# Kernel tuning notes

Measured on AMD Instinct MI355X. Metric: run time of the kernel, lower is better.

The kernel has to match this reference:

```python
import jax, jax.numpy as jnp
import numpy as np
import math

D = 768
H = 12
DH = D // H
L = 2
EPS = 1e-12
NEG = -10000.0


def layer_norm(x, w, b):
    u = jnp.mean(x, axis=-1, keepdims=True)
    s = jnp.mean((x - u) ** 2, axis=-1, keepdims=True)
    return w * ((x - u) / jnp.sqrt(s + EPS)) + b


def mha(q_in, k_in, v_in, mask, qw, qb, kw, kb, vw, vb):
    # q_in: (B,Lq,D); k_in/v_in: (B,Lk,D); mask: (B,Lq,Lk) or (B,1,Lk)
    B, Lq, _ = q_in.shape
    def proj(x, w, b):
        y = x @ w.T + b
        return y.reshape(x.shape[0], x.shape[1], H, DH).transpose(0, 2, 1, 3)
    q = proj(q_in, qw, qb)  # (B,H,Lq,DH)
    k = proj(k_in, kw, kb)
    v = proj(v_in, vw, vb)
    scores = jnp.einsum('bhqd,bhkd->bhqk', q, k) / math.sqrt(DH)
    scores = scores + (1.0 - mask[:, None]) * NEG  # additive mask, (B,1,Lq,Lk) broadcast
    probs = jax.nn.softmax(scores, axis=-1)
    ctx = jnp.einsum('bhqk,bhkd->bhqd', probs, v)
    return ctx.transpose(0, 2, 1, 3).reshape(B, Lq, D)


def setup_inputs() -> dict:
    key = jax.random.key(0)
    ks = jax.random.split(key, 8)
    B, Lt, Lv = 8, 1024, 512
    inp = {
        'dec_hidden_states': jax.random.normal(ks[0], (B, Lt, D), jnp.float32),
        'dec_mask': jnp.ones((B, Lt), jnp.float32),
        'enc_outputs': jax.random.normal(ks[1], (B, Lv, D), jnp.float32),
        'enc_mask': jnp.ones((B, Lv), jnp.float32),
    }
    wkeys = jax.random.split(ks[2], 7)
    names = ['sa_qw', 'sa_kw', 'sa_vw', 'ca_qw', 'ca_kw', 'ca_vw', 'out_w']
    for n, k in zip(names, wkeys):
        inp[n] = 0.02 * jax.random.normal(k, (L, D, D), jnp.float32)
    for n in ['sa_qb', 'sa_kb', 'sa_vb', 'ca_qb', 'ca_kb', 'ca_vb', 'out_b', 'n1_b', 'n2_b', 'n3_b']:
        inp[n] = jnp.zeros((L, D), jnp.float32)
    for n in ['n1_w', 'n2_w', 'n3_w']:
        inp[n] = jnp.ones((L, D), jnp.float32)
    return inp


def reference(dec_hidden_states, dec_mask, enc_outputs, enc_mask,
              sa_qw, sa_qb, sa_kw, sa_kb, sa_vw, sa_vb, n1_w, n1_b,
              ca_qw, ca_qb, ca_kw, ca_kb, ca_vw, ca_vb, n2_w, n2_b,
              out_w, out_b, n3_w, n3_b):
    Lt = dec_hidden_states.shape[1]
    causal = jnp.tril(jnp.ones((Lt, Lt), dec_mask.dtype))
    self_mask = dec_mask[:, None, :] * causal[None]        # (B,Lt,Lt)
    cross_mask = enc_mask[:, None, :]                      # (B,1,Lv)

    params = (sa_qw, sa_qb, sa_kw, sa_kb, sa_vw, sa_vb, n1_w, n1_b,
              ca_qw, ca_qb, ca_kw, ca_kb, ca_vw, ca_vb, n2_w, n2_b,
              out_w, out_b, n3_w, n3_b)

    def body(x, p):
        (qw, qb, kw, kb, vw, vb, w1, b1,
         cqw, cqb, ckw, ckb, cvw, cvb, w2, b2,
         ow, ob, w3, b3) = p
        a = mha(x, x, x, self_mask, qw, qb, kw, kb, vw, vb)
        x1 = layer_norm(a + x, w1, b1)
        c = mha(x1, enc_outputs, enc_outputs, cross_mask, cqw, cqb, ckw, ckb, cvw, cvb)
        x2 = layer_norm(x1 + c, w2, b2)
        # BertOutput called with (x2, x2): LN(dense(x2) + x2)
        y = layer_norm(x2 @ ow.T + ob + x2, w3, b3)
        return y, None

    out, _ = jax.lax.scan(body, dec_hidden_states, params)
    return out
```

## Files before the change

kernel.cpp:

```cpp
#include <hip/hip_runtime.h>
#include <hip/hip_bf16.h>

#define DMODEL 768
#define NH 12
#define DH 64
#define NEGC -10000.0f

#define AS1 __attribute__((address_space(1)))
#define AS3 __attribute__((address_space(3)))

typedef __bf16 bf16_t;
typedef __bf16 bf16x8 __attribute__((ext_vector_type(8)));
typedef float f32x4 __attribute__((ext_vector_type(4)));

__device__ __forceinline__ f32x4 mfma16(bf16x8 a, bf16x8 b, f32x4 c) {
    return __builtin_amdgcn_mfma_f32_16x16x32_bf16(a, b, c, 0, 0, 0);
}

__device__ __forceinline__ void gl_lds16(const bf16_t* g, void* l) {
    __builtin_amdgcn_global_load_lds((const AS1 void*)g, (AS3 void*)l, 16, 0, 0);
}

__global__ void probe_kernel(const unsigned int* m, int* flag) {
    *flag = (m[0] == 0x3F803F80u) ? 1 : 0;
}

__device__ __forceinline__ void cvt_group(const void* src, bf16_t* dst, int g, int isbf16) {
    if (isbf16) {
        ((bf16x8*)dst)[g] = ((const bf16x8*)src)[g];
    } else {
        const float* s = (const float*)src + (size_t)g * 8;
        bf16x8 v;
#pragma unroll
        for (int i = 0; i < 8; i++) v[i] = (bf16_t)s[i];
        ((bf16x8*)dst)[g] = v;
    }
}

__global__ __launch_bounds__(256) void cvt_kernel(const void* src, bf16_t* dst,
                                                  const int* flag, int n) {
    int g = blockIdx.x * 256 + threadIdx.x;
    if (g * 8 >= n) return;
    cvt_group(src, dst, g, *flag);
}

__global__ __launch_bounds__(256) void cvt7_kernel(
    const void* s0, const void* s1, const void* s2, const void* s3,
    const void* s4, const void* s5, const void* s6,
    bf16_t* dst, const int* flag)
{
    const void* srcs[7] = {s0, s1, s2, s3, s4, s5, s6};
    const void* src = srcs[blockIdx.y];
    bf16_t* d = dst + (size_t)blockIdx.y * 1179648;
    int g = blockIdx.x * 256 + threadIdx.x;
    cvt_group(src, d, g, *flag);
}

__global__ __launch_bounds__(256) void cvt13_kernel(
    const void* s0, const void* s1, const void* s2, const void* s3,
    const void* s4, const void* s5, const void* s6, const void* s7,
    const void* s8, const void* s9, const void* s10, const void* s11,
    const void* s12, bf16_t* dst, const int* flag)
{
    const void* srcs[13] = {s0, s1, s2, s3, s4, s5, s6, s7, s8, s9, s10, s11, s12};
    const void* src = srcs[blockIdx.x];
    bf16_t* d = dst + (size_t)blockIdx.x * 1536;
    int g = threadIdx.x;
    if (g >= 192) return;
    cvt_group(src, d, g, *flag);
}

__global__ __launch_bounds__(256, 4) void gemm128_kernel(
    const bf16_t* __restrict__ X0, const bf16_t* __restrict__ X1,
    const bf16_t* __restrict__ X2,
    const bf16_t* __restrict__ W0, const bf16_t* __restrict__ W1,
    const bf16_t* __restrict__ W2,
    const bf16_t* __restrict__ B0, const bf16_t* __restrict__ B1,
    const bf16_t* __restrict__ B2,
    bf16_t* __restrict__ O0, bf16_t* __restrict__ O1, bf16_t* __restrict__ O2,
    int nx, int ny0, int ny1, int ny2, int nz, int vz, int lkShift)
{
    __shared__ __attribute__((aligned(16))) bf16_t alds[2][128 * 32];
    __shared__ __attribute__((aligned(16))) bf16_t blds[2][128 * 32];

    const int tid  = threadIdx.x;
    const int lane = tid & 63;
    const int w    = tid >> 6;
    const int r    = lane & 15;
    const int q4   = lane >> 4;

    const int id     = blockIdx.x;
    const int xcd    = id & 7;
    const int slot   = id >> 3;
    const int planes = nx * nz;
    const int band   = xcd + 8 * (slot / planes);
    const int p      = slot % planes;
    const int z      = p / nx;
    const int bx     = p - z * nx;

    const int nyz = (z == 0) ? ny0 : ((z == 1) ? ny1 : ny2);
    if (band >= nyz) return;

    const int row0   = band * 128;
    const int col0   = bx * 128;
    const int wrow   = (w >> 1) * 64;
    const int wcol   = (w & 1) * 64;

    const bf16_t* X    = (z == 0) ? X0 : ((z == 1) ? X1 : X2);
    const bf16_t* W    = (z == 0) ? W0 : ((z == 1) ? W1 : W2);
    const bf16_t* bias = (z == 0) ? B0 : ((z == 1) ? B1 : B2);
    bf16_t*       out  = (z == 0) ? O0 : ((z == 1) ? O1 : O2);
    const int     mode = (z == vz) ? 1 : 0;

    const f32x4 zero4 = {0.f, 0.f, 0.f, 0.f};
    f32x4 acc[4][4];
#pragma unroll
    for (int i = 0; i < 4; i++)
#pragma unroll
        for (int j = 0; j < 4; j++) acc[i][j] = zero4;

    const int srow = w * 32 + (lane >> 2);
    const int sgc  = (lane & 3) ^ (srow & 3);
    const bf16_t* Xs = X + (size_t)(row0 + srow) * DMODEL + sgc * 8;
    const bf16_t* Ws = W + (size_t)(col0 + srow) * DMODEL + sgc * 8;

    auto stage = [&](int buf, int kb) {
#pragma unroll
        for (int j = 0; j < 2; j++) {
            gl_lds16(Xs + (size_t)(j * 16) * DMODEL + kb,
                     (char*)&alds[buf][0] + w * 2048 + j * 1024);
            gl_lds16(Ws + (size_t)(j * 16) * DMODEL + kb,
                     (char*)&blds[buf][0] + w * 2048 + j * 1024);
        }
    };

    const int NIT = DMODEL / 32;
    stage(0, 0);
    for (int i = 0; i < NIT; i++) {
        const int cur = i & 1;
        asm volatile("s_waitcnt lgkmcnt(0)" ::: "memory");
        __builtin_amdgcn_s_barrier();
        if (i + 1 < NIT) {
            stage(cur ^ 1, (i + 1) * 32);
            asm volatile("s_waitcnt vmcnt(4)" ::: "memory");
        } else {
            asm volatile("s_waitcnt vmcnt(0)" ::: "memory");
        }
        __builtin_amdgcn_s_barrier();

        const bf16_t* al = alds[cur];
        const bf16_t* bl = blds[cur];
        bf16x8 af[4], bf[4];
#pragma unroll
        for (int ii = 0; ii < 4; ii++) {
            int rr_ = wrow + ii * 16 + r;
            int pc  = q4 ^ (rr_ & 3);
            af[ii] = *(const bf16x8*)&al[rr_ * 32 + pc * 8];
        }
#pragma unroll
        for (int j = 0; j < 4; j++) {
            int cc_ = wcol + j * 16 + r;
            int pc  = q4 ^ (cc_ & 3);
            bf[j] = *(const bf16x8*)&bl[cc_ * 32 + pc * 8];
        }
#pragma unroll
        for (int ii = 0; ii < 4; ii++)
#pragma unroll
            for (int j = 0; j < 4; j++)
                acc[ii][j] = mfma16(af[ii], bf[j], acc[ii][j]);
    }

#pragma unroll
    for (int i = 0; i < 4; i++)
#pragma unroll
        for (int j = 0; j < 4; j++)
#pragma unroll
            for (int rr = 0; rr < 4; rr++) {
                int grow = row0 + wrow + i * 16 + q4 * 4 + rr;
                int gcol = col0 + wcol + j * 16 + r;
                float v = acc[i][j][rr] + (float)bias[gcol];
                if (mode == 0) {
                    out[(size_t)grow * DMODEL + gcol] = (bf16_t)v;
                } else {
                    int bidx = grow >> lkShift;
                    int t    = grow & ((1 << lkShift) - 1);
                    int h    = gcol >> 6;
                    int dd   = gcol & 63;
                    out[((size_t)((bidx * NH + h) * 64 + dd) << lkShift) + t] = (bf16_t)v;
                }
            }
}

__global__ __launch_bounds__(256) void attn_kernel(
    const bf16_t* Q, const bf16_t* __restrict__ K,
    const bf16_t* __restrict__ Vt, const bf16_t* __restrict__ mask,
    bf16_t* ctx, int Lq, int Lk, int causal)
{
    __shared__ __attribute__((aligned(16))) bf16_t kvlds[2][2][4096];
    __shared__ __attribute__((aligned(16))) bf16_t plds[4][1024];
    const int tid  = threadIdx.x;
    const int lane = tid & 63;
    const int wv   = tid >> 6;
    const int r    = lane & 15;
    const int q4   = lane >> 4;
    const int b    = blockIdx.z;
    const int h    = blockIdx.y;
    const int qblk = (gridDim.x - 1 - blockIdx.x) * 64;
    const int qbase = qblk + wv * 16;

    const bf16_t* Qp = Q + ((size_t)(b * Lq + qbase + r)) * DMODEL + h * DH + q4 * 8;
    bf16x8 qf0 = *(const bf16x8*)(Qp);
    bf16x8 qf1 = *(const bf16x8*)(Qp + 32);
    const bf16_t* Kg = K + ((size_t)b * Lk) * DMODEL + h * DH;
    const bf16_t* Vg = Vt + ((size_t)(b * NH + h) * DH) * Lk;
    const bf16_t* mp = mask + (size_t)b * Lk;

    const f32x4 zero4 = {0.f, 0.f, 0.f, 0.f};
    float psum[4] = {0.f, 0.f, 0.f, 0.f};
    f32x4 o[4] = {zero4, zero4, zero4, zero4};

    const int nt = causal ? ((qblk >> 6) + 1) : (Lk >> 6);

    auto stage = [&](int buf, int kb) {
#pragma unroll
        for (int j = 0; j < 2; j++) {
            gl_lds16(Kg + (size_t)(kb + wv * 16 + r) * DMODEL + (j * 4 + q4) * 8,
                     &kvlds[buf][0][wv * 1024 + j * 512]);
            gl_lds16(Vg + (size_t)(wv * 16 + r) * Lk + kb + (j * 4 + q4) * 8,
                     &kvlds[buf][1][wv * 1024 + j * 512]);
        }
    };

    stage(0, 0);
    for (int i = 0; i < nt; i++) {
        const int kb  = i << 6;
        const int cur = i & 1;
        asm volatile("s_waitcnt lgkmcnt(0)" ::: "memory");
        __builtin_amdgcn_s_barrier();
        float mb[4];
#pragma unroll
        for (int t = 0; t < 4; t++)
            mb[t] = (1.f - (float)mp[kb + t * 16 + r]) * NEGC;
        if (i + 1 < nt) {
            stage(cur ^ 1, kb + 64);
            asm volatile("s_waitcnt vmcnt(4)" ::: "memory");
        } else {
            asm volatile("s_waitcnt vmcnt(0)" ::: "memory");
        }
        __builtin_amdgcn_s_barrier();

        const bf16_t* kl = kvlds[cur][0];
        const bf16_t* vl = kvlds[cur][1];
        f32x4 s[4];
#pragma unroll
        for (int t = 0; t < 4; t++) {
            bf16x8 k0 = *(const bf16x8*)&kl[t * 1024 + lane * 8];
            bf16x8 k1 = *(const bf16x8*)&kl[t * 1024 + 512 + lane * 8];
            s[t] = mfma16(qf1, k1, mfma16(qf0, k0, zero4));
        }
#pragma unroll
        for (int t = 0; t < 4; t++) {
#pragma unroll
            for (int rr = 0; rr < 4; rr++) {
                float f = s[t][rr] * 0.125f + mb[t];
                float pv = __expf(f);
                if (causal && kb + t * 16 + r > qbase + q4 * 4 + rr) pv = 0.f;
                psum[rr] += pv;
                plds[wv][(t * 2 + (r >> 3)) * 128 + (q4 * 4 + rr) * 8 + (r & 7)] =
                    (bf16_t)pv;
            }
        }
        bf16x8 pa0 = *(const bf16x8*)&plds[wv][lane * 8];
        bf16x8 pa1 = *(const bf16x8*)&plds[wv][512 + lane * 8];
#pragma unroll
        for (int nc = 0; nc < 4; nc++) {
            bf16x8 v0 = *(const bf16x8*)&vl[nc * 1024 + lane * 8];
            bf16x8 v1 = *(const bf16x8*)&vl[nc * 1024 + 512 + lane * 8];
            o[nc] = mfma16(pa1, v1, mfma16(pa0, v0, o[nc]));
        }
    }

#pragma unroll
    for (int rr = 0; rr < 4; rr++) {
        psum[rr] += __shfl_xor(psum[rr], 1, 64);
        psum[rr] += __shfl_xor(psum[rr], 2, 64);
        psum[rr] += __shfl_xor(psum[rr], 4, 64);
        psum[rr] += __shfl_xor(psum[rr], 8, 64);
    }
#pragma unroll
    for (int nc = 0; nc < 4; nc++)
#pragma unroll
        for (int rr = 0; rr < 4; rr++) {
            int qi = qbase + q4 * 4 + rr;
            ctx[((size_t)(b * Lq + qi)) * DMODEL + h * DH + nc * 16 + r] =
                (bf16_t)(o[nc][rr] / psum[rr]);
        }
}

__global__ __launch_bounds__(256) void ln_kernel(
    const bf16_t* a, const bf16_t* res,
    const bf16_t* __restrict__ w, const bf16_t* __restrict__ b,
    void* out, int fin, const int* __restrict__ flag)
{
    __shared__ float red[8];
    const int row = blockIdx.x;
    const int tid = threadIdx.x;
    const int lane = tid & 63;
    const int wv = tid >> 6;
    const bf16_t* ap = a + (size_t)row * DMODEL;
    const bf16_t* rp = res + (size_t)row * DMODEL;
    const int outf32 = fin && (*flag == 0);

    float v[3];
#pragma unroll
    for (int i = 0; i < 3; i++) {
        int c = tid + i * 256;
        v[i] = (float)ap[c] + (float)rp[c];
    }
    float s = v[0] + v[1] + v[2];
#pragma unroll
    for (int m = 1; m < 64; m <<= 1) s += __shfl_xor(s, m, 64);
    if (lane == 0) red[wv] = s;
    __syncthreads();
    float u = (red[0] + red[1] + red[2] + red[3]) * (1.0f / DMODEL);
    float d0 = v[0] - u, d1 = v[1] - u, d2 = v[2] - u;
    float s2 = d0 * d0 + d1 * d1 + d2 * d2;
#pragma unroll
    for (int m = 1; m < 64; m <<= 1) s2 += __shfl_xor(s2, m, 64);
    if (lane == 0) red[4 + wv] = s2;
    __syncthreads();
    float var = (red[4] + red[5] + red[6] + red[7]) * (1.0f / DMODEL);
    float rstd = rsqrtf(var + 1e-12f);
#pragma unroll
    for (int i = 0; i < 3; i++) {
        int c = tid + i * 256;
        float y = ((v[i] - u) * rstd) * (float)w[c] + (float)b[c];
        if (outf32) ((float*)out)[(size_t)row * DMODEL + c] = y;
        else        ((bf16_t*)out)[(size_t)row * DMODEL + c] = (bf16_t)y;
    }
}

extern "C" void kernel_launch(void* const* d_in, const int* in_sizes, int n_in,
                              void* d_out, int out_size, void* d_ws, size_t ws_size,
                              hipStream_t stream)
{
    const int B = 8, Lt = 1024, Lv = 512;
    const size_t A = (size_t)B * Lt * DMODEL;
    const size_t E = (size_t)B * Lv * DMODEL;
    const size_t WT = 2 * (size_t)DMODEL * DMODEL;
    const int WSZ = DMODEL * DMODEL;

    char* p = (char*)d_ws;
    int* flagp = (int*)p;            p += 64;
    bf16_t* cdec = (bf16_t*)p;       p += A * 2;
    bf16_t* cenc = (bf16_t*)p;       p += E * 2;
    bf16_t* cdm  = (bf16_t*)p;       p += (size_t)B * Lt * 2;
    bf16_t* cem  = (bf16_t*)p;       p += (size_t)B * Lv * 2;
    bf16_t* cw   = (bf16_t*)p;       p += 7 * WT * 2;
    bf16_t* cb   = (bf16_t*)p;       p += 13 * 1536 * 2;
    bf16_t* b0   = (bf16_t*)p;       p += A * 2;
    bf16_t* b1   = (bf16_t*)p;       p += A * 2;
    bf16_t* b2   = (bf16_t*)p;       p += A * 2;
    bf16_t* dob  = (bf16_t*)d_out;

    const bf16_t* sa_qw = cw + 0 * WT, * sa_kw = cw + 1 * WT, * sa_vw = cw + 2 * WT;
    const bf16_t* ca_qw = cw + 3 * WT, * ca_kw = cw + 4 * WT, * ca_vw = cw + 5 * WT;
    const bf16_t* out_w = cw + 6 * WT;
    const bf16_t* sa_qb = cb + 0 * 1536, * sa_kb = cb + 1 * 1536, * sa_vb = cb + 2 * 1536;
    const bf16_t* ca_qb = cb + 3 * 1536, * ca_kb = cb + 4 * 1536, * ca_vb = cb + 5 * 1536;
    const bf16_t* out_b = cb + 6 * 1536;
    const bf16_t* n1_b  = cb + 7 * 1536, * n2_b = cb + 8 * 1536, * n3_b = cb + 9 * 1536;
    const bf16_t* n1_w  = cb + 10 * 1536, * n2_w = cb + 11 * 1536, * n3_w = cb + 12 * 1536;

    probe_kernel<<<1, 1, 0, stream>>>((const unsigned int*)d_in[1], flagp);
    cvt_kernel<<<dim3((unsigned)(A / 2048)), 256, 0, stream>>>(d_in[0], cdec, flagp, (int)A);
    cvt_kernel<<<dim3((unsigned)(E / 2048)), 256, 0, stream>>>(d_in[2], cenc, flagp, (int)E);
    cvt_kernel<<<dim3(4),  256, 0, stream>>>(d_in[1], cdm, flagp, B * Lt);
    cvt_kernel<<<dim3(2),  256, 0, stream>>>(d_in[3], cem, flagp, B * Lv);
    cvt7_kernel<<<dim3(576, 7), 256, 0, stream>>>(
        d_in[4], d_in[5], d_in[6], d_in[7], d_in[8], d_in[9], d_in[10], cw, flagp);
    cvt13_kernel<<<dim3(13), 256, 0, stream>>>(
        d_in[11], d_in[12], d_in[13], d_in[14], d_in[15], d_in[16], d_in[17],
        d_in[18], d_in[19], d_in[20], d_in[21], d_in[22], d_in[23], cb, flagp);

    dim3 blk(256);
    dim3 gQKV(6 * 64 * 3);
    dim3 gCrs(6 * 64 * 3);
    dim3 gOne(6 * 64 * 1);
    dim3 gAttn(Lt / 64, NH, B);
    dim3 gLN(B * Lt);

    for (int l = 0; l < 2; l++) {
        const bf16_t* xin = (l == 0) ? cdec : dob;
        gemm128_kernel<<<gQKV, blk, 0, stream>>>(
            xin, xin, xin,
            sa_qw + l * WSZ, sa_kw + l * WSZ, sa_vw + l * WSZ,
            sa_qb + l * DMODEL, sa_kb + l * DMODEL, sa_vb + l * DMODEL,
            b0, b1, b2, 6, 64, 64, 64, 3, 2, 10);
        attn_kernel<<<gAttn, blk, 0, stream>>>(b0, b1, b2, cdm, b0, Lt, Lt, 1);
        ln_kernel<<<gLN, blk, 0, stream>>>(b0, xin, n1_w + l * DMODEL, n1_b + l * DMODEL, b0, 0, flagp);
        gemm128_kernel<<<gCrs, blk, 0, stream>>>(
            b0, cenc, cenc,
            ca_qw + l * WSZ, ca_kw + l * WSZ, ca_vw + l * WSZ,
            ca_qb + l * DMODEL, ca_kb + l * DMODEL, ca_vb + l * DMODEL,
            b1, b2, dob, 6, 64, 32, 32, 3, 2, 9);
        attn_kernel<<<gAttn, blk, 0, stream>>>(b1, b2, dob, cem, b1, Lt, Lv, 0);
        ln_kernel<<<gLN, blk, 0, stream>>>(b1, b0, n2_w + l * DMODEL, n2_b + l * DMODEL, b1, 0, flagp);
        gemm128_kernel<<<gOne, blk, 0, stream>>>(
            b1, b1, b1,
            out_w + l * WSZ, out_w, out_w,
            out_b + l * DMODEL, out_b, out_b,
            b2, b2, b2, 6, 64, 64, 64, 1, -1, 0);
        ln_kernel<<<gLN, blk, 0, stream>>>(b2, b1, n3_w + l * DMODEL, n3_b + l * DMODEL, dob, (l == 1) ? 1 : 0, flagp);
    }
}
```

Before: 697.7 us.

## Enlarge GEMM tile to 256x128 with 512 threads, K=64 triple-buffered pipeline

Replaces the 128x128 GEMM with a 256x128 tile computed by 8 waves, a K-step of 64 and a three-deep LDS buffer that prefetches two stages ahead. The goal is more reuse of each loaded operand per tile, fewer barriers per K, and more load latency hidden behind compute. The transposed V output now goes out as packed 4-element vector stores. In exchange it uses much more LDS (about 144KB), which limits occupancy, and it launches half as many blocks. That leaves fewer waves to fill the CUs on these modest-sized GEMMs.

Result: faster. 665.9 us (-4.6%).

```diff
diff --git a/kernel.cpp b/kernel.cpp
--- a/kernel.cpp
+++ b/kernel.cpp
@@ -12,6 +12,7 @@
 typedef __bf16 bf16_t;
 typedef __bf16 bf16x8 __attribute__((ext_vector_type(8)));
 typedef float f32x4 __attribute__((ext_vector_type(4)));
+typedef unsigned int u32x2 __attribute__((ext_vector_type(2)));
 
 __device__ __forceinline__ f32x4 mfma16(bf16x8 a, bf16x8 b, f32x4 c) {
     return __builtin_amdgcn_mfma_f32_16x16x32_bf16(a, b, c, 0, 0, 0);
@@ -70,7 +71,7 @@
     cvt_group(src, d, g, *flag);
 }
 
-__global__ __launch_bounds__(256, 4) void gemm128_kernel(
+__global__ __launch_bounds__(512, 2) void gemm256x128_kernel(
     const bf16_t* __restrict__ X0, const bf16_t* __restrict__ X1,
     const bf16_t* __restrict__ X2,
     const bf16_t* __restrict__ W0, const bf16_t* __restrict__ W1,
@@ -80,8 +81,8 @@
     bf16_t* __restrict__ O0, bf16_t* __restrict__ O1, bf16_t* __restrict__ O2,
     int nx, int ny0, int ny1, int ny2, int nz, int vz, int lkShift)
 {
-    __shared__ __attribute__((aligned(16))) bf16_t alds[2][128 * 32];
-    __shared__ __attribute__((aligned(16))) bf16_t blds[2][128 * 32];
+    __shared__ __attribute__((aligned(16))) bf16_t alds[3][256 * 64];
+    __shared__ __attribute__((aligned(16))) bf16_t blds[3][128 * 64];
 
     const int tid  = threadIdx.x;
     const int lane = tid & 63;
@@ -101,10 +102,12 @@
     const int nyz = (z == 0) ? ny0 : ((z == 1) ? ny1 : ny2);
     if (band >= nyz) return;
 
-    const int row0   = band * 128;
-    const int col0   = bx * 128;
-    const int wrow   = (w >> 1) * 64;
-    const int wcol   = (w & 1) * 64;
+    const int row0 = band * 256;
+    const int col0 = bx * 128;
+    const int wr   = w >> 1;
+    const int wc   = w & 1;
+    const int wrow = wr * 64;
+    const int wcol = wc * 64;
 
     const bf16_t* X    = (z == 0) ? X0 : ((z == 1) ? X1 : X2);
     const bf16_t* W    = (z == 0) ? W0 : ((z == 1) ? W1 : W2);
@@ -119,30 +122,36 @@
 #pragma unroll
         for (int j = 0; j < 4; j++) acc[i][j] = zero4;
 
-    const int srow = w * 32 + (lane >> 2);
-    const int sgc  = (lane & 3) ^ (srow & 3);
-    const bf16_t* Xs = X + (size_t)(row0 + srow) * DMODEL + sgc * 8;
-    const bf16_t* Ws = W + (size_t)(col0 + srow) * DMODEL + sgc * 8;
+    const int srowA = w * 32 + (lane >> 3);
+    const int srowB = w * 16 + (lane >> 3);
+    const int sgcA  = (lane & 7) ^ (srowA & 7);
+    const int sgcB  = (lane & 7) ^ (srowB & 7);
+    const bf16_t* Xs = X + (size_t)(row0 + srowA) * DMODEL + sgcA * 8;
+    const bf16_t* Ws = W + (size_t)(col0 + srowB) * DMODEL + sgcB * 8;
 
     auto stage = [&](int buf, int kb) {
 #pragma unroll
-        for (int j = 0; j < 2; j++) {
-            gl_lds16(Xs + (size_t)(j * 16) * DMODEL + kb,
-                     (char*)&alds[buf][0] + w * 2048 + j * 1024);
-            gl_lds16(Ws + (size_t)(j * 16) * DMODEL + kb,
+        for (int j = 0; j < 4; j++)
+            gl_lds16(Xs + (size_t)(j * 8) * DMODEL + kb,
+                     (char*)&alds[buf][0] + w * 4096 + j * 1024);
+#pragma unroll
+        for (int j = 0; j < 2; j++)
+            gl_lds16(Ws + (size_t)(j * 8) * DMODEL + kb,
                      (char*)&blds[buf][0] + w * 2048 + j * 1024);
-        }
     };
 
-    const int NIT = DMODEL / 32;
+    const int NIT = DMODEL / 64;
     stage(0, 0);
+    stage(1, 64);
     for (int i = 0; i < NIT; i++) {
-        const int cur = i & 1;
+        const int cur = i % 3;
         asm volatile("s_waitcnt lgkmcnt(0)" ::: "memory");
         __builtin_amdgcn_s_barrier();
-        if (i + 1 < NIT) {
-            stage(cur ^ 1, (i + 1) * 32);
-            asm volatile("s_waitcnt vmcnt(4)" ::: "memory");
+        if (i + 2 < NIT) {
+            stage((i + 2) % 3, (i + 2) * 64);
+            asm volatile("s_waitcnt vmcnt(12)" ::: "memory");
+        } else if (i + 2 == NIT) {
+            asm volatile("s_waitcnt vmcnt(6)" ::: "memory");
         } else {
             asm volatile("s_waitcnt vmcnt(0)" ::: "memory");
         }
@@ -150,45 +159,55 @@
 
         const bf16_t* al = alds[cur];
         const bf16_t* bl = blds[cur];
-        bf16x8 af[4], bf[4];
-#pragma unroll
-        for (int ii = 0; ii < 4; ii++) {
-            int rr_ = wrow + ii * 16 + r;
-            int pc  = q4 ^ (rr_ & 3);
-            af[ii] = *(const bf16x8*)&al[rr_ * 32 + pc * 8];
-        }
+#pragma unroll
+        for (int ks = 0; ks < 2; ks++) {
+            bf16x8 af[4], bf[4];
+#pragma unroll
+            for (int ii = 0; ii < 4; ii++) {
+                int rr_ = wrow + ii * 16 + r;
+                int pc  = (ks * 4 + q4) ^ (rr_ & 7);
+                af[ii] = *(const bf16x8*)&al[rr_ * 64 + pc * 8];
+            }
+#pragma unroll
+            for (int j = 0; j < 4; j++) {
+                int cc_ = wcol + j * 16 + r;
+                int pc  = (ks * 4 + q4) ^ (cc_ & 7);
+                bf[j] = *(const bf16x8*)&bl[cc_ * 64 + pc * 8];
+            }
+#pragma unroll
+            for (int ii = 0; ii < 4; ii++)
+#pragma unroll
+                for (int j = 0; j < 4; j++)
+                    acc[ii][j] = mfma16(af[ii], bf[j], acc[ii][j]);
+        }
+    }
+
+#pragma unroll
+    for (int i = 0; i < 4; i++)
 #pragma unroll
         for (int j = 0; j < 4; j++) {
-            int cc_ = wcol + j * 16 + r;
-            int pc  = q4 ^ (cc_ & 3);
-            bf[j] = *(const bf16x8*)&bl[cc_ * 32 + pc * 8];
-        }
-#pragma unroll
-        for (int ii = 0; ii < 4; ii++)
-#pragma unroll
-            for (int j = 0; j < 4; j++)
-                acc[ii][j] = mfma16(af[ii], bf[j], acc[ii][j]);
-    }
-
-#pragma unroll
-    for (int i = 0; i < 4; i++)
-#pragma unroll
-        for (int j = 0; j < 4; j++)
-#pragma unroll
-            for (int rr = 0; rr < 4; rr++) {
-                int grow = row0 + wrow + i * 16 + q4 * 4 + rr;
-                int gcol = col0 + wcol + j * 16 + r;
-                float v = acc[i][j][rr] + (float)bias[gcol];
-                if (mode == 0) {
-                    out[(size_t)grow * DMODEL + gcol] = (bf16_t)v;
-                } else {
-                    int bidx = grow >> lkShift;
-                    int t    = grow & ((1 << lkShift) - 1);
-                    int h    = gcol >> 6;
-                    int dd   = gcol & 63;
-                    out[((size_t)((bidx * NH + h) * 64 + dd) << lkShift) + t] = (bf16_t)v;
+            int gcol = col0 + wcol + j * 16 + r;
+            float bv = (float)bias[gcol];
+            if (mode == 0) {
+#pragma unroll
+                for (int rr = 0; rr < 4; rr++) {
+                    int grow = row0 + wrow + i * 16 + q4 * 4 + rr;
+                    out[(size_t)grow * DMODEL + gcol] = (bf16_t)(acc[i][j][rr] + bv);
                 }
+            } else {
+                int growb = row0 + wrow + i * 16 + q4 * 4;
+                int bidx  = growb >> lkShift;
+                int t     = growb & ((1 << lkShift) - 1);
+                int h     = gcol >> 6;
+                int dd    = gcol & 63;
+                union { bf16_t h4[4]; u32x2 v; } pk;
+#pragma unroll
+                for (int rr = 0; rr < 4; rr++)
+                    pk.h4[rr] = (bf16_t)(acc[i][j][rr] + bv);
+                *reinterpret_cast<u32x2*>(
+                    &out[((size_t)((bidx * NH + h) * 64 + dd) << lkShift) + t]) = pk.v;
             }
+        }
 }
 
 __global__ __launch_bounds__(256) void attn_kernel(
@@ -383,34 +402,35 @@
         d_in[11], d_in[12], d_in[13], d_in[14], d_in[15], d_in[16], d_in[17],
         d_in[18], d_in[19], d_in[20], d_in[21], d_in[22], d_in[23], cb, flagp);
 
-    dim3 blk(256);
-    dim3 gQKV(6 * 64 * 3);
-    dim3 gCrs(6 * 64 * 3);
-    dim3 gOne(6 * 64 * 1);
+    dim3 blk256(256);
+    dim3 blk512(512);
+    dim3 gQKV(6 * 32 * 3);
+    dim3 gCrs(6 * 32 * 3);
+    dim3 gOut(6 * 32);
     dim3 gAttn(Lt / 64, NH, B);
     dim3 gLN(B * Lt);
 
     for (int l = 0; l < 2; l++) {
         const bf16_t* xin = (l == 0) ? cdec : dob;
-        gemm128_kernel<<<gQKV, blk, 0, stream>>>(
+        gemm256x128_kernel<<<gQKV, blk512, 0, stream>>>(
             xin, xin, xin,
             sa_qw + l * WSZ, sa_kw + l * WSZ, sa_vw + l * WSZ,
             sa_qb + l * DMODEL, sa_kb + l * DMODEL, sa_vb + l * DMODEL,
-            b0, b1, b2, 6, 64, 64, 64, 3, 2, 10);
-        attn_kernel<<<gAttn, blk, 0, stream>>>(b0, b1, b2, cdm, b0, Lt, Lt, 1);
-        ln_kernel<<<gLN, blk, 0, stream>>>(b0, xin, n1_w + l * DMODEL, n1_b + l * DMODEL, b0, 0, flagp);
-        gemm128_kernel<<<gCrs, blk, 0, stream>>>(
+            b0, b1, b2, 6, 32, 32, 32, 3, 2, 10);
+        attn_kernel<<<gAttn, blk256, 0, stream>>>(b0, b1, b2, cdm, b0, Lt, Lt, 1);
+        ln_kernel<<<gLN, blk256, 0, stream>>>(b0, xin, n1_w + l * DMODEL, n1_b + l * DMODEL, b0, 0, flagp);
+        gemm256x128_kernel<<<gCrs, blk512, 0, stream>>>(
             b0, cenc, cenc,
             ca_qw + l * WSZ, ca_kw + l * WSZ, ca_vw + l * WSZ,
             ca_qb + l * DMODEL, ca_kb + l * DMODEL, ca_vb + l * DMODEL,
-            b1, b2, dob, 6, 64, 32, 32, 3, 2, 9);
-        attn_kernel<<<gAttn, blk, 0, stream>>>(b1, b2, dob, cem, b1, Lt, Lv, 0);
-        ln_kernel<<<gLN, blk, 0, stream>>>(b1, b0, n2_w + l * DMODEL, n2_b + l * DMODEL, b1, 0, flagp);
-        gemm128_kernel<<<gOne, blk, 0, stream>>>(
+            b1, b2, dob, 6, 32, 16, 16, 3, 2, 9);
+        attn_kernel<<<gAttn, blk256, 0, stream>>>(b1, b2, dob, cem, b1, Lt, Lv, 0);
+        ln_kernel<<<gLN, blk256, 0, stream>>>(b1, b0, n2_w + l * DMODEL, n2_b + l * DMODEL, b1, 0, flagp);
+        gemm256x128_kernel<<<gOut, blk512, 0, stream>>>(
             b1, b1, b1,
             out_w + l * WSZ, out_w, out_w,
             out_b + l * DMODEL, out_b, out_b,
-            b2, b2, b2, 6, 64, 64, 64, 1, -1, 0);
-        ln_kernel<<<gLN, blk, 0, stream>>>(b2, b1, n3_w + l * DMODEL, n3_b + l * DMODEL, dob, (l == 1) ? 1 : 0, flagp);
-    }
-}
+            b2, b2, b2, 6, 32, 32, 32, 1, -1, 0);
+        ln_kernel<<<gLN, blk256, 0, stream>>>(b2, b1, n3_w + l * DMODEL, n3_b + l * DMODEL, dob, (l == 1) ? 1 : 0, flagp);
+    }
+}
```
